# Performance work log

Hardware: AMD Instinct MI355X
Metric: run time of the kernel (lower is better)

The kernel has to match this reference:

```python
import jax, jax.numpy as jnp
import numpy as np

B, L, D, H = 4, 1024, 1024, 16
HD = D // H  # head_dim = 64

def setup_inputs() -> dict:
    key = jax.random.key(0)
    ks = jax.random.split(key, 24)
    s = 1.0 / np.sqrt(D)
    sc = 1.0 / np.sqrt(12)
    inp = {
        "query": jax.random.normal(ks[0], (B, L, D), jnp.float32),
        "key": jax.random.normal(ks[1], (B, L, D), jnp.float32),
        "value": jax.random.normal(ks[2], (B, L, D), jnp.float32),
        "pitch_classes": jax.random.randint(ks[3], (L, 12), 0, 2, jnp.int32),
        "bass_onehot": jax.random.randint(ks[4], (L, 12), 0, 2, jnp.int32),
        "Wpq": jax.random.normal(ks[5], (D, D), jnp.float32) * s,
        "bpq": jnp.zeros((D,), jnp.float32),
        "Whq": jax.random.normal(ks[6], (D, D), jnp.float32) * s,
        "bhq": jnp.zeros((D,), jnp.float32),
        "Wvq": jax.random.normal(ks[7], (D, D), jnp.float32) * s,
        "bvq": jnp.zeros((D,), jnp.float32),
        "Wk": jax.random.normal(ks[8], (D, D), jnp.float32) * s,
        "bk": jnp.zeros((D,), jnp.float32),
        "Wv": jax.random.normal(ks[9], (D, D), jnp.float32) * s,
        "bv": jnp.zeros((D,), jnp.float32),
        "Wc": jax.random.normal(ks[10], (12, D), jnp.float32) * sc,
        "bc": jnp.zeros((D,), jnp.float32),
        "Wb": jax.random.normal(ks[11], (12, D), jnp.float32) * sc,
        "bb": jnp.zeros((D,), jnp.float32),
        "Wo": jax.random.normal(ks[12], (D, D), jnp.float32) * s,
        "bo": jnp.zeros((D,), jnp.float32),
    }
    return inp

def reference(query, key, value, pitch_classes, bass_onehot,
              Wpq, bpq, Whq, bhq, Wvq, bvq, Wk, bk, Wv, bv,
              Wc, bc, Wb, bb, Wo, bo):
    # projections (nn.Linear with weight stored as [in, out])
    pq = (query @ Wpq + bpq).reshape(B, L, H, HD)
    hq = (query @ Whq + bhq).reshape(B, L, H, HD)
    vq = (query @ Wvq + bvq).reshape(B, L, H, HD)
    k = (key @ Wk + bk).reshape(B, L, H, HD)
    v = (value @ Wv + bv).reshape(B, L, H, HD)
    # chord / bass features: per-position 0/1 12-dim vectors projected to D
    cf = (pitch_classes.astype(jnp.float32) @ Wc + bc).reshape(L, H, HD)
    bf = (bass_onehot.astype(jnp.float32) @ Wb + bb).reshape(L, H, HD)
    scale = HD ** -0.5
    pitch_scores = jnp.einsum('bqhd,bkhd->bhqk', pq, k)
    harmony_scores = jnp.einsum('bqhd,khd->bhqk', hq, cf)
    voice_scores = jnp.einsum('bqhd,khd->bhqk', vq, bf)
    scores = (pitch_scores + harmony_scores + voice_scores) * (scale / 3.0)
    attn = jax.nn.softmax(scores.astype(jnp.float32), axis=-1).astype(scores.dtype)
    context = jnp.einsum('bhqk,bkhd->bqhd', attn, v).reshape(B, L, D)
    output = context @ Wo + bo
    return output, attn
```

## Files before the change

kernel.cpp:

```cpp
#include <hip/hip_runtime.h>

#define B_ 4
#define L_ 1024
#define D_ 1024
#define H_ 16

typedef unsigned short u16;
typedef __attribute__((ext_vector_type(8))) short bf16x8;
typedef __attribute__((ext_vector_type(4))) float f32x4;

__device__ __forceinline__ u16 f2b(float x) {
  union { float f; unsigned u; } v; v.f = x;
  unsigned r = v.u + 0x7FFFu + ((v.u >> 16) & 1u);
  return (u16)(r >> 16);
}

__device__ __forceinline__ void gload_lds16(const void* g, void* lds) {
  __builtin_amdgcn_global_load_lds((const __attribute__((address_space(1))) void*)g,
                                   (__attribute__((address_space(3))) void*)lds, 16, 0, 0);
}

__global__ __launch_bounds__(256) void cast3_kernel(
    const float4* __restrict__ q, const float4* __restrict__ k, const float4* __restrict__ v,
    ushort4* __restrict__ qb, ushort4* __restrict__ kb, ushort4* __restrict__ vb) {
  int idx = blockIdx.x * 256 + threadIdx.x;
  float4 a = q[idx];
  qb[idx] = make_ushort4(f2b(a.x), f2b(a.y), f2b(a.z), f2b(a.w));
  a = k[idx];
  kb[idx] = make_ushort4(f2b(a.x), f2b(a.y), f2b(a.z), f2b(a.w));
  a = v[idx];
  vb[idx] = make_ushort4(f2b(a.x), f2b(a.y), f2b(a.z), f2b(a.w));
}

__global__ __launch_bounds__(256) void twt_kernel(
    const float* __restrict__ w0, const float* __restrict__ w1, const float* __restrict__ w2,
    const float* __restrict__ w3, const float* __restrict__ w4, const float* __restrict__ w5,
    u16* __restrict__ t0, u16* __restrict__ t1, u16* __restrict__ t2,
    u16* __restrict__ t3, u16* __restrict__ t4, u16* __restrict__ t5) {
  __shared__ float tile[32][33];
  const float* W; u16* T;
  switch (blockIdx.z) {
    case 0: W = w0; T = t0; break;
    case 1: W = w1; T = t1; break;
    case 2: W = w2; T = t2; break;
    case 3: W = w3; T = t3; break;
    case 4: W = w4; T = t4; break;
    default: W = w5; T = t5; break;
  }
  const int tx = threadIdx.x, ty = threadIdx.y;
  const int n0 = blockIdx.x * 32, k0 = blockIdx.y * 32;
#pragma unroll
  for (int jj = 0; jj < 4; ++jj)
    tile[ty + 8 * jj][tx] = W[(size_t)(k0 + ty + 8 * jj) * D_ + n0 + tx];
  __syncthreads();
#pragma unroll
  for (int jj = 0; jj < 4; ++jj)
    T[(size_t)(n0 + ty + 8 * jj) * D_ + k0 + tx] = f2b(tile[tx][ty + 8 * jj]);
}

__global__ __launch_bounds__(256) void chordfeat_kernel(
    const int* __restrict__ pitch, const int* __restrict__ bass,
    const float* __restrict__ Wc, const float* __restrict__ bc,
    const float* __restrict__ Wb, const float* __restrict__ bbias,
    u16* __restrict__ Kbig) {
  const int ll = blockIdx.x, t = threadIdx.x;
  __shared__ float pc[12], bs[12];
  if (t < 12) { pc[t] = (float)pitch[ll * 12 + t]; bs[t] = (float)bass[ll * 12 + t]; }
  __syncthreads();
  for (int n = t; n < D_; n += 256) {
    float c = bc[n], vv = bbias[n];
#pragma unroll
    for (int j = 0; j < 12; ++j) { c += pc[j] * Wc[j * D_ + n]; vv += bs[j] * Wb[j * D_ + n]; }
    const u16 cb = f2b(c), vb2 = f2b(vv);
    const int hh = n >> 6, d = n & 63;
#pragma unroll
    for (int b = 0; b < B_; ++b) {
      const size_t base = ((size_t)((b * H_ + hh) * L_ + ll)) * 192;
      Kbig[base + 64 + d] = cb;
      Kbig[base + 128 + d] = vb2;
    }
  }
}

__global__ __launch_bounds__(256) void proj_gemm_kernel(
    const u16* __restrict__ qb, const u16* __restrict__ kb, const u16* __restrict__ vb,
    const u16* __restrict__ WtQcat, const u16* __restrict__ WtK, const u16* __restrict__ WtV,
    const float* __restrict__ bpq, const float* __restrict__ bhq, const float* __restrict__ bvq,
    const float* __restrict__ bk, const float* __restrict__ bv,
    u16* __restrict__ Qbig, u16* __restrict__ Kbig, u16* __restrict__ VtD) {
  __shared__ u16 lA[128 * 32];
  __shared__ u16 lB[128 * 32];
  int bid = blockIdx.x;
  const u16 *A, *Bt; const float* bias; u16* dst; int n0, m0, mode;
  if (bid < 768) {
    A = qb; Bt = WtQcat; dst = Qbig; mode = 0;
    n0 = (bid % 24) * 128; m0 = (bid / 24) * 128;
    const int seg = n0 >> 10;
    bias = seg == 0 ? bpq : (seg == 1 ? bhq : bvq);
  } else if (bid < 1024) {
    bid -= 768;
    A = kb; Bt = WtK; bias = bk; dst = Kbig; mode = 0;
    n0 = (bid % 8) * 128; m0 = (bid / 8) * 128;
  } else {
    bid -= 1024;
    A = vb; Bt = WtV; bias = bv; dst = VtD; mode = 1;
    n0 = (bid % 8) * 128; m0 = (bid / 8) * 128;
  }
  const int t = threadIdx.x;
  const int w = t >> 6, l = t & 63;
  const int wm = w >> 1, wn = w & 1;
  const int lr = l & 15, lg = l >> 4;
  f32x4 acc[4][4];
#pragma unroll
  for (int i = 0; i < 4; ++i)
#pragma unroll
    for (int j = 0; j < 4; ++j)
      acc[i][j] = (f32x4){0.f, 0.f, 0.f, 0.f};

  const int r0 = t >> 2, c0 = t & 3;

  for (int k0 = 0; k0 < 1024; k0 += 32) {
    gload_lds16(A + (size_t)(m0 + r0) * 1024 + k0 + c0 * 8, &lA[w * 512]);
    gload_lds16(A + (size_t)(m0 + 64 + r0) * 1024 + k0 + c0 * 8, &lA[2048 + w * 512]);
    gload_lds16(Bt + (size_t)(n0 + r0) * 1024 + k0 + c0 * 8, &lB[w * 512]);
    gload_lds16(Bt + (size_t)(n0 + 64 + r0) * 1024 + k0 + c0 * 8, &lB[2048 + w * 512]);
    __syncthreads();
    bf16x8 af[4], bfr[4];
#pragma unroll
    for (int i = 0; i < 4; ++i) {
      af[i]  = *(const bf16x8*)&lA[(wm * 64 + i * 16 + lr) * 32 + lg * 8];
      bfr[i] = *(const bf16x8*)&lB[(wn * 64 + i * 16 + lr) * 32 + lg * 8];
    }
#pragma unroll
    for (int i = 0; i < 4; ++i)
#pragma unroll
      for (int j = 0; j < 4; ++j)
        acc[i][j] = __builtin_amdgcn_mfma_f32_16x16x32_bf16(af[i], bfr[j], acc[i][j], 0, 0, 0);
    __syncthreads();
  }

#pragma unroll
  for (int i = 0; i < 4; ++i) {
    const int mb = m0 + wm * 64 + i * 16 + lg * 4;
    const int b = mb >> 10, qq = mb & 1023;
#pragma unroll
    for (int j = 0; j < 4; ++j) {
      const int n = n0 + wn * 64 + j * 16 + lr;
      const float bvv = bias[n & 1023];
      if (mode == 0) {
        const int seg = n >> 10, hh = (n & 1023) >> 6, d = n & 63;
        const size_t base = ((size_t)((b * H_ + hh) * L_ + qq)) * 192 + seg * 64 + d;
#pragma unroll
        for (int r = 0; r < 4; ++r)
          dst[base + (size_t)r * 192] = f2b(acc[i][j][r] + bvv);
      } else {
        const int hh = n >> 6, d = n & 63;
        ushort4 pk = make_ushort4(f2b(acc[i][j][0] + bvv), f2b(acc[i][j][1] + bvv),
                                  f2b(acc[i][j][2] + bvv), f2b(acc[i][j][3] + bvv));
        *(ushort4*)&dst[((size_t)((b * H_ + hh) * 64 + d)) * 1024 + qq] = pk;
      }
    }
  }
}

__global__ __launch_bounds__(256) void out_gemm_kernel(
    const u16* __restrict__ A, const u16* __restrict__ Bt,
    const float* __restrict__ bias, float* __restrict__ dst) {
  __shared__ u16 lA[128 * 32];
  __shared__ u16 lB[128 * 32];
  const int t = threadIdx.x;
  const int w = t >> 6, l = t & 63;
  const int wm = w >> 1, wn = w & 1;
  const int lr = l & 15, lg = l >> 4;
  const int m0 = blockIdx.y * 128, n0 = blockIdx.x * 128;
  f32x4 acc[4][4];
#pragma unroll
  for (int i = 0; i < 4; ++i)
#pragma unroll
    for (int j = 0; j < 4; ++j)
      acc[i][j] = (f32x4){0.f, 0.f, 0.f, 0.f};
  const int r0 = t >> 2, c0 = t & 3;
  for (int k0 = 0; k0 < 1024; k0 += 32) {
    gload_lds16(A + (size_t)(m0 + r0) * 1024 + k0 + c0 * 8, &lA[w * 512]);
    gload_lds16(A + (size_t)(m0 + 64 + r0) * 1024 + k0 + c0 * 8, &lA[2048 + w * 512]);
    gload_lds16(Bt + (size_t)(n0 + r0) * 1024 + k0 + c0 * 8, &lB[w * 512]);
    gload_lds16(Bt + (size_t)(n0 + 64 + r0) * 1024 + k0 + c0 * 8, &lB[2048 + w * 512]);
    __syncthreads();
    bf16x8 af[4], bfr[4];
#pragma unroll
    for (int i = 0; i < 4; ++i) {
      af[i]  = *(const bf16x8*)&lA[(wm * 64 + i * 16 + lr) * 32 + lg * 8];
      bfr[i] = *(const bf16x8*)&lB[(wn * 64 + i * 16 + lr) * 32 + lg * 8];
    }
#pragma unroll
    for (int i = 0; i < 4; ++i)
#pragma unroll
      for (int j = 0; j < 4; ++j)
        acc[i][j] = __builtin_amdgcn_mfma_f32_16x16x32_bf16(af[i], bfr[j], acc[i][j], 0, 0, 0);
    __syncthreads();
  }
#pragma unroll
  for (int i = 0; i < 4; ++i) {
    const int mb = m0 + wm * 64 + i * 16 + lg * 4;
#pragma unroll
    for (int j = 0; j < 4; ++j) {
      const int n = n0 + wn * 64 + j * 16 + lr;
      const float bvv = bias[n];
#pragma unroll
      for (int r = 0; r < 4; ++r)
        dst[(size_t)(mb + r) * 1024 + n] = acc[i][j][r] + bvv;
    }
  }
}

__global__ __launch_bounds__(256) void attn_kernel(
    const u16* __restrict__ Qbig, const u16* __restrict__ Kbig, const u16* __restrict__ Vt,
    float* __restrict__ attn_out, u16* __restrict__ ctx) {
  __shared__ u16 Plds[16][1032];
  __shared__ float red[2][4][16];
  const int qt = blockIdx.x, h = blockIdx.y, b = blockIdx.z;
  const int bh = b * H_ + h;
  const int q0 = qt * 16;
  const int t = threadIdx.x, w = t >> 6, l = t & 63;
  const int lr = l & 15, lg = l >> 4;

  bf16x8 aq[6];
  {
    const u16* Qrow = Qbig + ((size_t)bh * L_ + q0 + lr) * 192 + lg * 8;
#pragma unroll
    for (int c = 0; c < 6; ++c) aq[c] = *(const bf16x8*)(Qrow + c * 32);
  }

  const float scl = 1.0f / 24.0f;
  float s[16][4];
#pragma unroll
  for (int kt = 0; kt < 16; ++kt) {
    const int kp0 = w * 256 + kt * 16;
    const u16* Krow = Kbig + ((size_t)bh * L_ + kp0 + lr) * 192 + lg * 8;
    f32x4 acc = (f32x4){0.f, 0.f, 0.f, 0.f};
#pragma unroll
    for (int c = 0; c < 6; ++c) {
      const bf16x8 kf = *(const bf16x8*)(Krow + c * 32);
      acc = __builtin_amdgcn_mfma_f32_16x16x32_bf16(kf, aq[c], acc, 0, 0, 0);
    }
#pragma unroll
    for (int r = 0; r < 4; ++r) s[kt][r] = acc[r] * scl;
  }

  float mx = -1e30f;
#pragma unroll
  for (int kt = 0; kt < 16; ++kt)
#pragma unroll
    for (int r = 0; r < 4; ++r) mx = fmaxf(mx, s[kt][r]);
  mx = fmaxf(mx, __shfl_xor(mx, 16));
  mx = fmaxf(mx, __shfl_xor(mx, 32));
  if (lg == 0) red[0][w][lr] = mx;
  __syncthreads();
  mx = fmaxf(fmaxf(red[0][0][lr], red[0][1][lr]), fmaxf(red[0][2][lr], red[0][3][lr]));
  float sum = 0.f;
#pragma unroll
  for (int kt = 0; kt < 16; ++kt)
#pragma unroll
    for (int r = 0; r < 4; ++r) { s[kt][r] = __expf(s[kt][r] - mx); sum += s[kt][r]; }
  sum += __shfl_xor(sum, 16);
  sum += __shfl_xor(sum, 32);
  if (lg == 0) red[1][w][lr] = sum;
  __syncthreads();
  const float inv = 1.0f / (red[1][0][lr] + red[1][1][lr] + red[1][2][lr] + red[1][3][lr]);

  float* aout = attn_out + ((size_t)bh * L_ + q0 + lr) * L_ + w * 256 + lg * 4;
#pragma unroll
  for (int kt = 0; kt < 16; ++kt) {
    const float p0 = s[kt][0] * inv, p1 = s[kt][1] * inv;
    const float p2 = s[kt][2] * inv, p3 = s[kt][3] * inv;
    *(float4*)(aout + kt * 16) = make_float4(p0, p1, p2, p3);
    *(ushort4*)&Plds[lr][w * 256 + kt * 16 + lg * 4] =
        make_ushort4(f2b(p0), f2b(p1), f2b(p2), f2b(p3));
  }
  __syncthreads();

  {
    const int dw = w * 16;
    const u16* Vrow = Vt + ((size_t)bh * 64 + dw + lr) * L_ + lg * 8;
    f32x4 acc = (f32x4){0.f, 0.f, 0.f, 0.f};
#pragma unroll
    for (int cc = 0; cc < 32; ++cc) {
      const bf16x8 pf = *(const bf16x8*)&Plds[lr][cc * 32 + lg * 8];
      const bf16x8 vf = *(const bf16x8*)(Vrow + cc * 32);
      acc = __builtin_amdgcn_mfma_f32_16x16x32_bf16(pf, vf, acc, 0, 0, 0);
    }
#pragma unroll
    for (int r = 0; r < 4; ++r)
      ctx[((size_t)(b * L_ + q0 + lg * 4 + r)) * D_ + h * 64 + dw + lr] = f2b(acc[r]);
  }
}

extern "C" void kernel_launch(void* const* d_in, const int* in_sizes, int n_in,
                              void* d_out, int out_size, void* d_ws, size_t ws_size,
                              hipStream_t stream) {
  (void)in_sizes; (void)n_in; (void)out_size; (void)ws_size;
  const float* q   = (const float*)d_in[0];
  const float* k   = (const float*)d_in[1];
  const float* v   = (const float*)d_in[2];
  const int* pitch = (const int*)d_in[3];
  const int* bass  = (const int*)d_in[4];
  const float* Wpq = (const float*)d_in[5];  const float* bpq  = (const float*)d_in[6];
  const float* Whq = (const float*)d_in[7];  const float* bhq  = (const float*)d_in[8];
  const float* Wvq = (const float*)d_in[9];  const float* bvq  = (const float*)d_in[10];
  const float* Wk  = (const float*)d_in[11]; const float* bk   = (const float*)d_in[12];
  const float* Wv  = (const float*)d_in[13]; const float* bv   = (const float*)d_in[14];
  const float* Wc  = (const float*)d_in[15]; const float* bc   = (const float*)d_in[16];
  const float* Wb  = (const float*)d_in[17]; const float* bbias= (const float*)d_in[18];
  const float* Wo  = (const float*)d_in[19]; const float* bo   = (const float*)d_in[20];

  char* ws = (char*)d_ws;
  const size_t MB = 1024 * 1024;
  u16* qb   = (u16*)(ws + 0 * MB);
  u16* kb   = (u16*)(ws + 8 * MB);
  u16* vb   = (u16*)(ws + 16 * MB);
  u16* WtPQ = (u16*)(ws + 24 * MB);
  u16* WtHQ = (u16*)(ws + 26 * MB);
  u16* WtVQ = (u16*)(ws + 28 * MB);
  u16* WtK  = (u16*)(ws + 30 * MB);
  u16* WtV  = (u16*)(ws + 32 * MB);
  u16* WtO  = (u16*)(ws + 34 * MB);
  u16* Qbig = (u16*)(ws + 36 * MB);
  u16* Kbig = (u16*)(ws + 60 * MB);
  u16* Vt   = (u16*)(ws + 84 * MB);
  u16* ctx  = (u16*)(ws + 92 * MB);

  float* out  = (float*)d_out;
  float* attn = out + (size_t)B_ * L_ * D_;

  cast3_kernel<<<dim3(4096), dim3(256), 0, stream>>>(
      (const float4*)q, (const float4*)k, (const float4*)v,
      (ushort4*)qb, (ushort4*)kb, (ushort4*)vb);
  twt_kernel<<<dim3(32, 32, 6), dim3(32, 8), 0, stream>>>(
      Wpq, Whq, Wvq, Wk, Wv, Wo, WtPQ, WtHQ, WtVQ, WtK, WtV, WtO);
  chordfeat_kernel<<<dim3(1024), dim3(256), 0, stream>>>(pitch, bass, Wc, bc, Wb, bbias, Kbig);
  proj_gemm_kernel<<<dim3(1280), dim3(256), 0, stream>>>(
      qb, kb, vb, WtPQ, WtK, WtV, bpq, bhq, bvq, bk, bv, Qbig, Kbig, Vt);
  attn_kernel<<<dim3(64, 16, 4), dim3(256), 0, stream>>>(Qbig, Kbig, Vt, attn, ctx);
  out_gemm_kernel<<<dim3(8, 32), dim3(256), 0, stream>>>(ctx, WtO, bo, out);
}
```

Baseline: 731.8 us.

## Restructure attention into two-pass streaming with LDS-staged double-buffered K/V tiles

```diff
diff --git a/kernel.cpp b/kernel.cpp
--- a/kernel.cpp
+++ b/kernel.cpp
@@ -216,83 +216,134 @@
 __global__ __launch_bounds__(256) void attn_kernel(
     const u16* __restrict__ Qbig, const u16* __restrict__ Kbig, const u16* __restrict__ Vt,
     float* __restrict__ attn_out, u16* __restrict__ ctx) {
-  __shared__ u16 Plds[16][1032];
-  __shared__ float red[2][4][16];
+  __shared__ u16 Kl[2][32 * 192];
+  __shared__ u16 Vl[2][64 * 32];
+  __shared__ u16 Pl[4][16 * 40];
   const int qt = blockIdx.x, h = blockIdx.y, b = blockIdx.z;
   const int bh = b * H_ + h;
-  const int q0 = qt * 16;
-  const int t = threadIdx.x, w = t >> 6, l = t & 63;
+  const int q0 = qt * 64;
+  const int t = threadIdx.x, wq = t >> 6, l = t & 63;
   const int lr = l & 15, lg = l >> 4;
 
   bf16x8 aq[6];
   {
-    const u16* Qrow = Qbig + ((size_t)bh * L_ + q0 + lr) * 192 + lg * 8;
+    const u16* Qrow = Qbig + ((size_t)bh * L_ + q0 + wq * 16 + lr) * 192 + lg * 8;
 #pragma unroll
     for (int c = 0; c < 6; ++c) aq[c] = *(const bf16x8*)(Qrow + c * 32);
   }
 
+  const u16* Kbase = Kbig + (size_t)bh * L_ * 192;
+  const u16* Vbase = Vt + (size_t)bh * 64 * L_;
+
+  int ksrc[3];
+#pragma unroll
+  for (int i = 0; i < 3; ++i) {
+    const int off = (wq * 3 + i) * 1024 + l * 16;
+    const int row = off / 384;
+    const int col = off - row * 384;
+    ksrc[i] = row * 192 + (((col ^ ((row & 7) << 4))) >> 1);
+  }
+  const int voff = wq * 1024 + l * 16;
+  const int vd = voff >> 6, vcol = (voff & 63) >> 1;
+
   const float scl = 1.0f / 24.0f;
-  float s[16][4];
-#pragma unroll
-  for (int kt = 0; kt < 16; ++kt) {
-    const int kp0 = w * 256 + kt * 16;
-    const u16* Krow = Kbig + ((size_t)bh * L_ + kp0 + lr) * 192 + lg * 8;
-    f32x4 acc = (f32x4){0.f, 0.f, 0.f, 0.f};
+  float m = -1e30f, lden = 0.f;
+
+  int csw[6];
+#pragma unroll
+  for (int c = 0; c < 6; ++c) csw[c] = (c * 32 + lg * 8) ^ ((lr & 7) << 3);
+
+#pragma unroll
+  for (int i = 0; i < 3; ++i)
+    gload_lds16(Kbase + ksrc[i], &Kl[0][(wq * 3 + i) * 512]);
+  __syncthreads();
+
+  for (int ti = 0; ti < 32; ++ti) {
+    const int cur = ti & 1;
+    if (ti < 31) {
+#pragma unroll
+      for (int i = 0; i < 3; ++i)
+        gload_lds16(Kbase + (size_t)(ti + 1) * 32 * 192 + ksrc[i],
+                    &Kl[cur ^ 1][(wq * 3 + i) * 512]);
+    }
+    f32x4 a0 = (f32x4){0.f, 0.f, 0.f, 0.f}, a1 = (f32x4){0.f, 0.f, 0.f, 0.f};
 #pragma unroll
     for (int c = 0; c < 6; ++c) {
-      const bf16x8 kf = *(const bf16x8*)(Krow + c * 32);
-      acc = __builtin_amdgcn_mfma_f32_16x16x32_bf16(kf, aq[c], acc, 0, 0, 0);
-    }
-#pragma unroll
-    for (int r = 0; r < 4; ++r) s[kt][r] = acc[r] * scl;
-  }
-
-  float mx = -1e30f;
-#pragma unroll
-  for (int kt = 0; kt < 16; ++kt)
-#pragma unroll
-    for (int r = 0; r < 4; ++r) mx = fmaxf(mx, s[kt][r]);
-  mx = fmaxf(mx, __shfl_xor(mx, 16));
-  mx = fmaxf(mx, __shfl_xor(mx, 32));
-  if (lg == 0) red[0][w][lr] = mx;
+      const bf16x8 k0 = *(const bf16x8*)&Kl[cur][lr * 192 + csw[c]];
+      const bf16x8 k1 = *(const bf16x8*)&Kl[cur][(16 + lr) * 192 + csw[c]];
+      a0 = __builtin_amdgcn_mfma_f32_16x16x32_bf16(k0, aq[c], a0, 0, 0, 0);
+      a1 = __builtin_amdgcn_mfma_f32_16x16x32_bf16(k1, aq[c], a1, 0, 0, 0);
+    }
+    float tm = fmaxf(fmaxf(fmaxf(a0[0], a0[1]), fmaxf(a0[2], a0[3])),
+                     fmaxf(fmaxf(a1[0], a1[1]), fmaxf(a1[2], a1[3]))) * scl;
+    tm = fmaxf(tm, __shfl_xor(tm, 16));
+    tm = fmaxf(tm, __shfl_xor(tm, 32));
+    const float mn = fmaxf(m, tm);
+    float ps = __expf(a0[0] * scl - mn) + __expf(a0[1] * scl - mn) +
+               __expf(a0[2] * scl - mn) + __expf(a0[3] * scl - mn) +
+               __expf(a1[0] * scl - mn) + __expf(a1[1] * scl - mn) +
+               __expf(a1[2] * scl - mn) + __expf(a1[3] * scl - mn);
+    ps += __shfl_xor(ps, 16);
+    ps += __shfl_xor(ps, 32);
+    lden = lden * __expf(m - mn) + ps;
+    m = mn;
+    __syncthreads();
+  }
+
+  const float invl = 1.0f / lden;
+
+#pragma unroll
+  for (int i = 0; i < 3; ++i)
+    gload_lds16(Kbase + ksrc[i], &Kl[0][(wq * 3 + i) * 512]);
+  gload_lds16(Vbase + (size_t)vd * L_ + vcol, &Vl[0][wq * 512]);
   __syncthreads();
-  mx = fmaxf(fmaxf(red[0][0][lr], red[0][1][lr]), fmaxf(red[0][2][lr], red[0][3][lr]));
-  float sum = 0.f;
-#pragma unroll
-  for (int kt = 0; kt < 16; ++kt)
-#pragma unroll
-    for (int r = 0; r < 4; ++r) { s[kt][r] = __expf(s[kt][r] - mx); sum += s[kt][r]; }
-  sum += __shfl_xor(sum, 16);
-  sum += __shfl_xor(sum, 32);
-  if (lg == 0) red[1][w][lr] = sum;
-  __syncthreads();
-  const float inv = 1.0f / (red[1][0][lr] + red[1][1][lr] + red[1][2][lr] + red[1][3][lr]);
-
-  float* aout = attn_out + ((size_t)bh * L_ + q0 + lr) * L_ + w * 256 + lg * 4;
-#pragma unroll
-  for (int kt = 0; kt < 16; ++kt) {
-    const float p0 = s[kt][0] * inv, p1 = s[kt][1] * inv;
-    const float p2 = s[kt][2] * inv, p3 = s[kt][3] * inv;
-    *(float4*)(aout + kt * 16) = make_float4(p0, p1, p2, p3);
-    *(ushort4*)&Plds[lr][w * 256 + kt * 16 + lg * 4] =
-        make_ushort4(f2b(p0), f2b(p1), f2b(p2), f2b(p3));
-  }
-  __syncthreads();
-
-  {
-    const int dw = w * 16;
-    const u16* Vrow = Vt + ((size_t)bh * 64 + dw + lr) * L_ + lg * 8;
-    f32x4 acc = (f32x4){0.f, 0.f, 0.f, 0.f};
-#pragma unroll
-    for (int cc = 0; cc < 32; ++cc) {
-      const bf16x8 pf = *(const bf16x8*)&Plds[lr][cc * 32 + lg * 8];
-      const bf16x8 vf = *(const bf16x8*)(Vrow + cc * 32);
-      acc = __builtin_amdgcn_mfma_f32_16x16x32_bf16(pf, vf, acc, 0, 0, 0);
-    }
+
+  f32x4 opv[4];
+#pragma unroll
+  for (int dc = 0; dc < 4; ++dc) opv[dc] = (f32x4){0.f, 0.f, 0.f, 0.f};
+  u16* Pw = &Pl[wq][0];
+  float* arow = attn_out + ((size_t)bh * L_ + q0 + wq * 16 + lr) * L_;
+
+  for (int ti = 0; ti < 32; ++ti) {
+    const int cur = ti & 1;
+    if (ti < 31) {
+#pragma unroll
+      for (int i = 0; i < 3; ++i)
+        gload_lds16(Kbase + (size_t)(ti + 1) * 32 * 192 + ksrc[i],
+                    &Kl[cur ^ 1][(wq * 3 + i) * 512]);
+      gload_lds16(Vbase + (size_t)vd * L_ + (ti + 1) * 32 + vcol, &Vl[cur ^ 1][wq * 512]);
+    }
+    f32x4 a0 = (f32x4){0.f, 0.f, 0.f, 0.f}, a1 = (f32x4){0.f, 0.f, 0.f, 0.f};
+#pragma unroll
+    for (int c = 0; c < 6; ++c) {
+      const bf16x8 k0 = *(const bf16x8*)&Kl[cur][lr * 192 + csw[c]];
+      const bf16x8 k1 = *(const bf16x8*)&Kl[cur][(16 + lr) * 192 + csw[c]];
+      a0 = __builtin_amdgcn_mfma_f32_16x16x32_bf16(k0, aq[c], a0, 0, 0, 0);
+      a1 = __builtin_amdgcn_mfma_f32_16x16x32_bf16(k1, aq[c], a1, 0, 0, 0);
+    }
+    const float p0 = __expf(a0[0] * scl - m) * invl, p1 = __expf(a0[1] * scl - m) * invl;
+    const float p2 = __expf(a0[2] * scl - m) * invl, p3 = __expf(a0[3] * scl - m) * invl;
+    const float p4 = __expf(a1[0] * scl - m) * invl, p5 = __expf(a1[1] * scl - m) * invl;
+    const float p6 = __expf(a1[2] * scl - m) * invl, p7 = __expf(a1[3] * scl - m) * invl;
+    *(float4*)(arow + ti * 32 + lg * 4) = make_float4(p0, p1, p2, p3);
+    *(float4*)(arow + ti * 32 + 16 + lg * 4) = make_float4(p4, p5, p6, p7);
+    *(ushort4*)&Pw[lr * 40 + lg * 4] = make_ushort4(f2b(p0), f2b(p1), f2b(p2), f2b(p3));
+    *(ushort4*)&Pw[lr * 40 + 16 + lg * 4] = make_ushort4(f2b(p4), f2b(p5), f2b(p6), f2b(p7));
+    const bf16x8 pf = *(const bf16x8*)&Pw[lr * 40 + lg * 8];
+#pragma unroll
+    for (int dc = 0; dc < 4; ++dc) {
+      const bf16x8 vf = *(const bf16x8*)&Vl[cur][(dc * 16 + lr) * 32 + lg * 8];
+      opv[dc] = __builtin_amdgcn_mfma_f32_16x16x32_bf16(pf, vf, opv[dc], 0, 0, 0);
+    }
+    __syncthreads();
+  }
+
+#pragma unroll
+  for (int dc = 0; dc < 4; ++dc)
 #pragma unroll
     for (int r = 0; r < 4; ++r)
-      ctx[((size_t)(b * L_ + q0 + lg * 4 + r)) * D_ + h * 64 + dw + lr] = f2b(acc[r]);
-  }
+      ctx[((size_t)(b * L_ + q0 + wq * 16 + lg * 4 + r)) * D_ + h * 64 + dc * 16 + lr] =
+          f2b(opv[dc][r]);
 }
 
 extern "C" void kernel_launch(void* const* d_in, const int* in_sizes, int n_in,
@@ -340,6 +391,6 @@
   chordfeat_kernel<<<dim3(1024), dim3(256), 0, stream>>>(pitch, bass, Wc, bc, Wb, bbias, Kbig);
   proj_gemm_kernel<<<dim3(1280), dim3(256), 0, stream>>>(
       qb, kb, vb, WtPQ, WtK, WtV, bpq, bhq, bvq, bk, bv, Qbig, Kbig, Vt);
-  attn_kernel<<<dim3(64, 16, 4), dim3(256), 0, stream>>>(Qbig, Kbig, Vt, attn, ctx);
+  attn_kernel<<<dim3(16, 16, 4), dim3(256), 0, stream>>>(Qbig, Kbig, Vt, attn, ctx);
   out_gemm_kernel<<<dim3(8, 32), dim3(256), 0, stream>>>(ctx, WtO, bo, out);
 }
```

Measured after the change: 586.5 us. 19.9% less time.
